# Kernel tuning notes

Measured on AMD Instinct MI355X. Metric: run time of the kernel, lower is better.

The kernel has to match this reference:

```python
import jax, jax.numpy as jnp
import numpy as np

B = 128        # batch
N = 4096       # FLAGS.network_node
D_IN = 32      # embedding_in_size
D_OUT = 32     # embedding_out_size


def setup_inputs() -> dict:
    key = jax.random.key(0)
    k1, k2, k3, k4 = jax.random.split(key, 4)
    inputs = jax.random.normal(k1, (B, N * D_IN), dtype=jnp.float32)
    # mean-aggregation neighbor matrix: random nonneg, row-normalized (get_neibhour_nodes_matrix_mean)
    raw = jax.random.uniform(k2, (N, N), dtype=jnp.float32)
    adj = raw / jnp.sum(raw, axis=1, keepdims=True)
    # glorot uniform init as in source
    r = np.sqrt(6.0 / (D_IN + D_OUT)).astype(np.float32)
    W_neigh = jax.random.uniform(k3, (D_IN, D_OUT), minval=-r, maxval=r, dtype=jnp.float32)
    W_self = jax.random.uniform(k4, (D_IN, D_OUT), minval=-r, maxval=r, dtype=jnp.float32)
    return {"inputs": inputs, "adj": adj, "W_neigh": W_neigh, "W_self": W_self, "batch_train": 0}


def reference(inputs, adj, W_neigh, W_self, batch_train):
    # Math: relu(x @ (I_N (x) W_self + A (x) W_neigh))
    # Kronecker vec-trick: reshape x to [B, N, D_IN]; then
    #   x @ (A (x) W) reshaped = einsum('bip,ij,pq->bjq', x3, A, W)
    x3 = inputs.reshape(B, N, D_IN)
    self_part = jnp.einsum('bnp,pq->bnq', x3, W_self)            # I_N (x) W_self
    tmp = jnp.einsum('bip,pq->biq', x3, W_neigh)                  # apply small weight first
    neigh_part = jnp.einsum('biq,ij->bjq', tmp, adj)              # aggregate over graph
    out = jax.nn.relu(self_part + neigh_part)
    return out.reshape(B, N * D_OUT)
```

## Files before the change

### kernel.cpp

```cpp
#include <hip/hip_runtime.h>
#include <hip/hip_bf16.h>

#define N_NODES 4096
#define BATCH   128
#define DD      32

typedef float  f32x4  __attribute__((ext_vector_type(4)));
typedef __bf16 bf16x8 __attribute__((ext_vector_type(8)));
typedef int    i32x4  __attribute__((ext_vector_type(4)));
typedef int    i32x8  __attribute__((ext_vector_type(8)));

#define PREP_BLOCKS 2048
#define TR_BLOCKS   4096

__device__ __forceinline__ void async_copy16(const void* g, void* l) {
    __builtin_amdgcn_global_load_lds(
        (const __attribute__((address_space(1))) unsigned int*)g,
        (__attribute__((address_space(3))) unsigned int*)l,
        16, 0, 0);
}

__device__ __forceinline__ unsigned pack_fp8x4(float a, float b, float c, float d) {
    int v = __builtin_amdgcn_cvt_pk_fp8_f32(a, b, 0, false);
    v     = __builtin_amdgcn_cvt_pk_fp8_f32(c, d, v, true);
    return (unsigned)v;
}

__global__ __launch_bounds__(256) void k_pre(
    const float* __restrict__ x, const float* __restrict__ adj,
    const float* __restrict__ Wn, const float* __restrict__ Ws,
    unsigned char* __restrict__ T8, unsigned char* __restrict__ adjT8,
    float* __restrict__ out)
{
    __shared__ float ts[64][65];
    const int tid = threadIdx.x;

    if (blockIdx.x < PREP_BLOCKS) {
        const int lane = tid & 63;
        const int gw   = (blockIdx.x * 256 + tid) >> 6;
        const int m    = lane & 15;
        const int quad = lane >> 4;

        bf16x8 bn[2], bs[2];
#pragma unroll
        for (int h = 0; h < 2; ++h) {
            const int n = m + h * 16;
#pragma unroll
            for (int j = 0; j < 8; ++j) {
                const int k = quad * 8 + j;
                bn[h][j] = (__bf16)Wn[k * 32 + n];
                bs[h][j] = (__bf16)Ws[k * 32 + n];
            }
        }

        for (int t = gw; t < 32768; t += 8192) {
            const int row0 = t << 4;
            const int b    = row0 >> 12;
            const int i0   = row0 & 4095;

            const float4* xp = (const float4*)(x + (size_t)(row0 + m) * DD + quad * 8);
            const float4 x0 = xp[0], x1 = xp[1];
            bf16x8 a;
            a[0] = (__bf16)x0.x; a[1] = (__bf16)x0.y; a[2] = (__bf16)x0.z; a[3] = (__bf16)x0.w;
            a[4] = (__bf16)x1.x; a[5] = (__bf16)x1.y; a[6] = (__bf16)x1.z; a[7] = (__bf16)x1.w;

            const f32x4 z = {};
            const f32x4 cT0 = __builtin_amdgcn_mfma_f32_16x16x32_bf16(a, bn[0], z, 0, 0, 0);
            const f32x4 cT1 = __builtin_amdgcn_mfma_f32_16x16x32_bf16(a, bn[1], z, 0, 0, 0);
            const f32x4 cU0 = __builtin_amdgcn_mfma_f32_16x16x32_bf16(a, bs[0], z, 0, 0, 0);
            const f32x4 cU1 = __builtin_amdgcn_mfma_f32_16x16x32_bf16(a, bs[1], z, 0, 0, 0);

            *(unsigned*)&T8[((size_t)(b * 32 + m))      * N_NODES + i0 + quad * 4] =
                pack_fp8x4(cT0[0], cT0[1], cT0[2], cT0[3]);
            *(unsigned*)&T8[((size_t)(b * 32 + m + 16)) * N_NODES + i0 + quad * 4] =
                pack_fp8x4(cT1[0], cT1[1], cT1[2], cT1[3]);

            float* ub = out + (size_t)b * (N_NODES * DD) + (size_t)(i0 + quad * 4) * DD;
#pragma unroll
            for (int r = 0; r < 4; ++r) {
                ub[r * DD + m]      = cU0[r];
                ub[r * DD + m + 16] = cU1[r];
            }
        }
    } else {
        const int bid = blockIdx.x - PREP_BLOCKS;
        const int cx  = tid & 63;
        const int cy  = tid >> 6;
        const int i0  = (bid >> 6) << 6;
        const int j0  = (bid & 63) << 6;
#pragma unroll
        for (int r = 0; r < 16; ++r) {
            const int row = cy * 16 + r;
            ts[row][cx] = adj[(size_t)(i0 + row) * N_NODES + j0 + cx];
        }
        __syncthreads();
        const int il = (tid & 7) * 8;
        const int jb = tid >> 3;
#pragma unroll
        for (int rr = 0; rr < 2; ++rr) {
            const int jl = jb + rr * 32;
            float v[8];
#pragma unroll
            for (int k = 0; k < 8; ++k) v[k] = ts[il + k][jl] * 4096.0f;
            uint2 p;
            p.x = pack_fp8x4(v[0], v[1], v[2], v[3]);
            p.y = pack_fp8x4(v[4], v[5], v[6], v[7]);
            *(uint2*)&adjT8[(size_t)(j0 + jl) * N_NODES + i0 + il] = p;
        }
    }
}

__global__ __launch_bounds__(256) void k_gemm_neigh(
    const unsigned char* __restrict__ A8,
    const unsigned char* __restrict__ B8,
    float* __restrict__ out)
{
    __shared__ alignas(16) unsigned char As[128 * 128];
    __shared__ alignas(16) unsigned char Bs[128 * 128];

    const int tid   = threadIdx.x;
    const int lane  = tid & 63;
    const int wave  = tid >> 6;
    const int bm    = blockIdx.y << 7;
    const int bn    = blockIdx.x << 7;
    const int waveM = (wave >> 1) << 6;
    const int waveN = (wave & 1) << 6;
    const int lr    = lane & 15;
    const int lq    = lane >> 4;
    const int sw    = lr & 7;

    f32x4 acc[4][4] = {};

    const int srow = tid >> 3;
    const int scol = ((tid & 7) ^ (srow & 7)) * 16;
    const unsigned char* ga = A8 + (size_t)(bm + srow) * 4096 + scol;
    const unsigned char* gb = B8 + (size_t)(bn + srow) * 4096 + scol;
    char* la = (char*)As + tid * 16;
    char* lb = (char*)Bs + tid * 16;

    for (int k0 = 0; k0 < 4096; k0 += 128) {
#pragma unroll
        for (int n = 0; n < 4; ++n) {
            async_copy16(ga + (size_t)(n * 32) * 4096 + k0, la + n * 4096);
            async_copy16(gb + (size_t)(n * 32) * 4096 + k0, lb + n * 4096);
        }
        __syncthreads();

        i32x8 af[4], bfr[4];
#pragma unroll
        for (int t = 0; t < 4; ++t) {
            const int ra = (waveM + t * 16 + lr) * 128;
            const int rb = (waveN + t * 16 + lr) * 128;
            const int c0 = ((2 * lq)     ^ sw) * 16;
            const int c1 = ((2 * lq + 1) ^ sw) * 16;
            const i32x4 alo = *(const i32x4*)&As[ra + c0];
            const i32x4 ahi = *(const i32x4*)&As[ra + c1];
            const i32x4 blo = *(const i32x4*)&Bs[rb + c0];
            const i32x4 bhi = *(const i32x4*)&Bs[rb + c1];
            af[t][0]=alo[0]; af[t][1]=alo[1]; af[t][2]=alo[2]; af[t][3]=alo[3];
            af[t][4]=ahi[0]; af[t][5]=ahi[1]; af[t][6]=ahi[2]; af[t][7]=ahi[3];
            bfr[t][0]=blo[0]; bfr[t][1]=blo[1]; bfr[t][2]=blo[2]; bfr[t][3]=blo[3];
            bfr[t][4]=bhi[0]; bfr[t][5]=bhi[1]; bfr[t][6]=bhi[2]; bfr[t][7]=bhi[3];
        }
#pragma unroll
        for (int tm = 0; tm < 4; ++tm)
#pragma unroll
            for (int tn = 0; tn < 4; ++tn)
                acc[tm][tn] = __builtin_amdgcn_mfma_scale_f32_16x16x128_f8f6f4(
                    af[tm], bfr[tn], acc[tm][tn],
                    0, 0,
                    0, 0x7F,
                    0, 0x73);
        __syncthreads();
    }

#pragma unroll
    for (int tm = 0; tm < 4; ++tm) {
        const int gm0 = bm + waveM + tm * 16 + lq * 4;
        const int b   = gm0 >> 5;
        const int q0  = gm0 & 31;
#pragma unroll
        for (int tn = 0; tn < 4; ++tn) {
            const int gj = bn + waveN + tn * 16 + lr;
            float* p = out + (size_t)b * (N_NODES * DD) + (size_t)gj * DD + q0;
            const float4 u = *(const float4*)p;
            float4 v;
            v.x = fmaxf(acc[tm][tn][0] + u.x, 0.0f);
            v.y = fmaxf(acc[tm][tn][1] + u.y, 0.0f);
            v.z = fmaxf(acc[tm][tn][2] + u.z, 0.0f);
            v.w = fmaxf(acc[tm][tn][3] + u.w, 0.0f);
            *(float4*)p = v;
        }
    }
}

extern "C" void kernel_launch(void* const* d_in, const int* in_sizes, int n_in,
                              void* d_out, int out_size, void* d_ws, size_t ws_size,
                              hipStream_t stream) {
    const float* x   = (const float*)d_in[0];
    const float* adj = (const float*)d_in[1];
    const float* Wn  = (const float*)d_in[2];
    const float* Ws  = (const float*)d_in[3];
    float* out = (float*)d_out;

    unsigned char* T8    = (unsigned char*)d_ws;
    unsigned char* adjT8 = T8 + (size_t)N_NODES * N_NODES;

    hipLaunchKernelGGL(k_pre, dim3(PREP_BLOCKS + TR_BLOCKS), dim3(256), 0, stream,
                       x, adj, Wn, Ws, T8, adjT8, out);
    hipLaunchKernelGGL(k_gemm_neigh, dim3(32, 32), dim3(256), 0, stream, T8, adjT8, out);
}
```

Baseline: 273.4 us.

## Triple-buffer FP8 GEMM with 256x128 tiles and swizzled block order

Rewrites the neighbour GEMM to use 256x128 output tiles per workgroup with a three-stage LDS ring of async global-to-LDS copies. Explicit vmcnt waits plus a single barrier per k-step replace the load/sync/compute/sync pattern, so loads for step t+2 overlap compute on step t. Blocks are remapped through a 1D grid with interleaved ordering to improve L2 reuse. This costs 144KB of LDS and 128 accumulator registers per thread, which forces one workgroup per CU and halves the grid to 512 blocks, a risk for occupancy and load balance across CUs.

```diff
diff --git a/kernel.cpp b/kernel.cpp
--- a/kernel.cpp
+++ b/kernel.cpp
@@ -110,85 +110,114 @@
     }
 }
 
-__global__ __launch_bounds__(256) void k_gemm_neigh(
+__global__ __launch_bounds__(256, 1) void k_gemm_neigh(
     const unsigned char* __restrict__ A8,
     const unsigned char* __restrict__ B8,
     float* __restrict__ out)
 {
-    __shared__ alignas(16) unsigned char As[128 * 128];
-    __shared__ alignas(16) unsigned char Bs[128 * 128];
+    __shared__ alignas(16) unsigned char As[3 * 256 * 128];
+    __shared__ alignas(16) unsigned char Bs[3 * 128 * 128];
 
     const int tid   = threadIdx.x;
     const int lane  = tid & 63;
     const int wave  = tid >> 6;
-    const int bm    = blockIdx.y << 7;
-    const int bn    = blockIdx.x << 7;
-    const int waveM = (wave >> 1) << 6;
-    const int waveN = (wave & 1) << 6;
     const int lr    = lane & 15;
     const int lq    = lane >> 4;
     const int sw    = lr & 7;
-
-    f32x4 acc[4][4] = {};
-
-    const int srow = tid >> 3;
-    const int scol = ((tid & 7) ^ (srow & 7)) * 16;
-    const unsigned char* ga = A8 + (size_t)(bm + srow) * 4096 + scol;
-    const unsigned char* gb = B8 + (size_t)(bn + srow) * 4096 + scol;
-    char* la = (char*)As + tid * 16;
-    char* lb = (char*)Bs + tid * 16;
-
-    for (int k0 = 0; k0 < 4096; k0 += 128) {
-#pragma unroll
-        for (int n = 0; n < 4; ++n) {
-            async_copy16(ga + (size_t)(n * 32) * 4096 + k0, la + n * 4096);
-            async_copy16(gb + (size_t)(n * 32) * 4096 + k0, lb + n * 4096);
-        }
-        __syncthreads();
-
-        i32x8 af[4], bfr[4];
-#pragma unroll
-        for (int t = 0; t < 4; ++t) {
-            const int ra = (waveM + t * 16 + lr) * 128;
-            const int rb = (waveN + t * 16 + lr) * 128;
-            const int c0 = ((2 * lq)     ^ sw) * 16;
-            const int c1 = ((2 * lq + 1) ^ sw) * 16;
-            const i32x4 alo = *(const i32x4*)&As[ra + c0];
-            const i32x4 ahi = *(const i32x4*)&As[ra + c1];
-            const i32x4 blo = *(const i32x4*)&Bs[rb + c0];
-            const i32x4 bhi = *(const i32x4*)&Bs[rb + c1];
-            af[t][0]=alo[0]; af[t][1]=alo[1]; af[t][2]=alo[2]; af[t][3]=alo[3];
-            af[t][4]=ahi[0]; af[t][5]=ahi[1]; af[t][6]=ahi[2]; af[t][7]=ahi[3];
-            bfr[t][0]=blo[0]; bfr[t][1]=blo[1]; bfr[t][2]=blo[2]; bfr[t][3]=blo[3];
-            bfr[t][4]=bhi[0]; bfr[t][5]=bhi[1]; bfr[t][6]=bhi[2]; bfr[t][7]=bhi[3];
-        }
-#pragma unroll
-        for (int tm = 0; tm < 4; ++tm)
-#pragma unroll
-            for (int tn = 0; tn < 4; ++tn)
-                acc[tm][tn] = __builtin_amdgcn_mfma_scale_f32_16x16x128_f8f6f4(
-                    af[tm], bfr[tn], acc[tm][tn],
+    const int waveM = ((wave >> 1) & 1) * 128;
+    const int waveN = (wave & 1) * 64;
+
+    const int wg = (blockIdx.x & 7) * 64 + (blockIdx.x >> 3);
+    const int Mb = (wg >> 5) << 8;
+    const int Nb = (wg & 31) << 7;
+
+    const int    srow = tid >> 3;
+    const int    scol = ((tid & 7) ^ (srow & 7)) * 16;
+    const size_t aoff = (size_t)(Mb + srow) * 4096 + scol;
+    const size_t boff = (size_t)(Nb + srow) * 4096 + scol;
+    char* const  lA   = (char*)As + tid * 16;
+    char* const  lB   = (char*)Bs + tid * 16;
+
+    f32x4 acc[8][4] = {};
+
+#define STAGE(bufi, k0)                                                      \
+    {                                                                        \
+        _Pragma("unroll")                                                    \
+        for (int n = 0; n < 8; ++n)                                          \
+            async_copy16(A8 + aoff + (size_t)(n * 32) * 4096 + (k0),         \
+                         lA + (bufi) * 32768 + n * 4096);                    \
+        _Pragma("unroll")                                                    \
+        for (int n = 0; n < 4; ++n)                                          \
+            async_copy16(B8 + boff + (size_t)(n * 32) * 4096 + (k0),         \
+                         lB + (bufi) * 16384 + n * 4096);                    \
+    }
+
+    STAGE(0, 0);
+    STAGE(1, 128);
+    asm volatile("s_waitcnt vmcnt(12)" ::: "memory");
+    __builtin_amdgcn_s_barrier();
+
+    for (int t = 0; t < 32; ++t) {
+        const int bc = t % 3;
+        if (t + 2 < 32) {
+            const int bs = (t + 2) % 3;
+            STAGE(bs, (t + 2) * 128);
+        }
+
+        const unsigned char* const Ab = As + bc * 32768;
+        const unsigned char* const Bb = Bs + bc * 16384;
+        const int c0 = ((2 * lq)     ^ sw) * 16;
+        const int c1 = ((2 * lq + 1) ^ sw) * 16;
+
+        i32x8 bf[4];
+#pragma unroll
+        for (int fn = 0; fn < 4; ++fn) {
+            const int rb = (waveN + fn * 16 + lr) * 128;
+            const i32x4 blo = *(const i32x4*)&Bb[rb + c0];
+            const i32x4 bhi = *(const i32x4*)&Bb[rb + c1];
+            bf[fn][0]=blo[0]; bf[fn][1]=blo[1]; bf[fn][2]=blo[2]; bf[fn][3]=blo[3];
+            bf[fn][4]=bhi[0]; bf[fn][5]=bhi[1]; bf[fn][6]=bhi[2]; bf[fn][7]=bhi[3];
+        }
+#pragma unroll
+        for (int fm = 0; fm < 8; ++fm) {
+            const int ra = (waveM + fm * 16 + lr) * 128;
+            const i32x4 alo = *(const i32x4*)&Ab[ra + c0];
+            const i32x4 ahi = *(const i32x4*)&Ab[ra + c1];
+            i32x8 af;
+            af[0]=alo[0]; af[1]=alo[1]; af[2]=alo[2]; af[3]=alo[3];
+            af[4]=ahi[0]; af[5]=ahi[1]; af[6]=ahi[2]; af[7]=ahi[3];
+#pragma unroll
+            for (int fn = 0; fn < 4; ++fn)
+                acc[fm][fn] = __builtin_amdgcn_mfma_scale_f32_16x16x128_f8f6f4(
+                    af, bf[fn], acc[fm][fn],
                     0, 0,
                     0, 0x7F,
                     0, 0x73);
-        __syncthreads();
-    }
-
-#pragma unroll
-    for (int tm = 0; tm < 4; ++tm) {
-        const int gm0 = bm + waveM + tm * 16 + lq * 4;
+        }
+
+        if (t + 1 < 32) {
+            if (t + 2 < 32) { asm volatile("s_waitcnt vmcnt(12)" ::: "memory"); }
+            else            { asm volatile("s_waitcnt vmcnt(0)"  ::: "memory"); }
+            __builtin_amdgcn_s_barrier();
+        }
+    }
+#undef STAGE
+
+#pragma unroll
+    for (int fm = 0; fm < 8; ++fm) {
+        const int gm0 = Mb + waveM + fm * 16 + lq * 4;
         const int b   = gm0 >> 5;
         const int q0  = gm0 & 31;
 #pragma unroll
-        for (int tn = 0; tn < 4; ++tn) {
-            const int gj = bn + waveN + tn * 16 + lr;
+        for (int fn = 0; fn < 4; ++fn) {
+            const int gj = Nb + waveN + fn * 16 + lr;
             float* p = out + (size_t)b * (N_NODES * DD) + (size_t)gj * DD + q0;
             const float4 u = *(const float4*)p;
             float4 v;
-            v.x = fmaxf(acc[tm][tn][0] + u.x, 0.0f);
-            v.y = fmaxf(acc[tm][tn][1] + u.y, 0.0f);
-            v.z = fmaxf(acc[tm][tn][2] + u.z, 0.0f);
-            v.w = fmaxf(acc[tm][tn][3] + u.w, 0.0f);
+            v.x = fmaxf(acc[fm][fn][0] + u.x, 0.0f);
+            v.y = fmaxf(acc[fm][fn][1] + u.y, 0.0f);
+            v.z = fmaxf(acc[fm][fn][2] + u.z, 0.0f);
+            v.w = fmaxf(acc[fm][fn][3] + u.w, 0.0f);
             *(float4*)p = v;
         }
     }
@@ -208,5 +237,5 @@
 
     hipLaunchKernelGGL(k_pre, dim3(PREP_BLOCKS + TR_BLOCKS), dim3(256), 0, stream,
                        x, adj, Wn, Ws, T8, adjT8, out);
-    hipLaunchKernelGGL(k_gemm_neigh, dim3(32, 32), dim3(256), 0, stream, T8, adjT8, out);
-}
+    hipLaunchKernelGGL(k_gemm_neigh, dim3(512), dim3(256), 0, stream, T8, adjT8, out);
+}
```

New measurement: 307.0 us. 1.12x slower.
